# Kernel optimization log

Hardware: AMD Instinct MI355X
Metric: run time of the kernel (lower is better)

The kernel has to match this reference:

```python
import jax, jax.numpy as jnp
import numpy as np

N_SAMPLES = 32768   # exp.n_samples = 2**15
N_FRAMES = 128      # exp.n_frames = n_samples // 256
N_EVENTS = 16
MODEL_DIM = 128
N_FREQS = 16        # 2*16 + 1 = 33 pos-encoding features
POS_DIM = 2 * N_FREQS + 1


def pos_encoded(n_frames, n_freqs):
    # linear position in [-pi, pi] plus sin/cos at geometrically spaced freqs
    x = np.linspace(-np.pi, np.pi, n_frames, dtype=np.float32)[:, None]
    feats = [x]
    for i in range(n_freqs):
        feats.append(np.sin((2.0 ** i) * x))
        feats.append(np.cos((2.0 ** i) * x))
    return jnp.asarray(np.concatenate(feats, axis=-1))  # (n_frames, 33)


def hard_softmax_st(x):
    # softmax -> one-hot at argmax (value forced to exactly 1.0), straight-through backward
    sm = jax.nn.softmax(x, axis=-1)
    onehot = jax.nn.one_hot(jnp.argmax(sm, axis=-1), x.shape[-1], dtype=x.dtype)
    return sm + jax.lax.stop_gradient(onehot - sm)


def fft_convolve(env, tf):
    n = env.shape[-1]
    env = jnp.pad(env, ((0, 0), (0, 0), (0, n)))
    tf = jnp.pad(tf, ((0, 0), (0, 0), (0, n)))
    spec = jnp.fft.rfft(env, axis=-1, norm='ortho') * jnp.fft.rfft(tf, axis=-1, norm='ortho')
    return jnp.fft.irfft(spec, axis=-1, norm='ortho')[..., :n]


def setup_inputs() -> dict:
    key = jax.random.key(0)
    k1, k2, k3, k4, k5 = jax.random.split(key, 5)
    B = 32
    time_latent = jax.random.normal(k1, (B * N_EVENTS, MODEL_DIM), jnp.float32)
    stems = jax.random.normal(k2, (B, N_EVENTS, N_SAMPLES), jnp.float32)
    targets = jax.random.normal(k3, (B, N_EVENTS, N_SAMPLES), jnp.float32)
    lim = 1.0 / np.sqrt(MODEL_DIM)
    W = jax.random.uniform(k4, (MODEL_DIM, POS_DIM), jnp.float32, -lim, lim)
    b = jax.random.uniform(k5, (POS_DIM,), jnp.float32, -lim, lim)
    return {"time_latent": time_latent, "stems": stems, "targets": targets, "W": W, "b": b}


def reference(time_latent, stems, targets, W, b):
    # to_pos linear projection: (B*E, 128) -> (B*E, 33)
    p = time_latent @ W + b
    p = p / (jnp.linalg.norm(p, axis=-1, keepdims=True) + 1e-8)
    pos = pos_encoded(N_FRAMES, N_FREQS)
    pos = pos / (jnp.linalg.norm(pos, axis=-1, keepdims=True) + 1e-8)
    sim = p @ pos.T                      # (B*E, n_frames)
    sm = hard_softmax_st(sim)            # one-hot forward, softmax backward
    step = N_SAMPLES // N_FRAMES         # 256
    sparse = jnp.zeros((p.shape[0], N_SAMPLES), p.dtype).at[:, ::step].set(sm)
    sparse = sparse.reshape(-1, N_EVENTS, N_SAMPLES)  # (B, 16, 32768)
    return fft_convolve(sparse, stems)
```

## Files before the change

kernel.cpp:

```cpp
#include <hip/hip_runtime.h>
#include <math.h>

#define N_SAMPLES 32768
#define N_FRAMES  128
#define N_EVENTS  16
#define MODEL_DIM 128
#define N_FREQS   16
#define POS_DIM   33
#define N_ROWS    512
#define SPLIT     4


__global__ __launch_bounds__(64) void pos_kernel(float* __restrict__ pos_hat) {
    int f = blockIdx.x;
    int j = threadIdx.x;

    __shared__ float s_feat[POS_DIM];
    __shared__ float s_inv;

    double step = (2.0 * M_PI) / 127.0;
    double xd = -M_PI + (double)f * step;
    if (f == N_FRAMES - 1) xd = M_PI;
    float x = (float)xd;

    if (j < POS_DIM) {
        float v;
        if (j == 0) {
            v = x;
        } else {
            int i = (j - 1) >> 1;
            double arg = ldexp((double)x, i);
            v = (j & 1) ? (float)sin(arg) : (float)cos(arg);
        }
        s_feat[j] = v;
    }
    __syncthreads();

    if (j == 0) {
        double nrm = 0.0;
        for (int k = 0; k < POS_DIM; ++k)
            nrm += (double)s_feat[k] * (double)s_feat[k];
        s_inv = 1.0f / ((float)sqrt(nrm) + 1e-8f);
    }
    __syncthreads();

    if (j < POS_DIM) pos_hat[f * POS_DIM + j] = s_feat[j] * s_inv;
}

__global__ __launch_bounds__(1024) void fused_kernel(
    const float* __restrict__ tl,
    const float* __restrict__ W,
    const float* __restrict__ b,
    const float* __restrict__ pos_hat,
    const float* __restrict__ stems,
    float*       __restrict__ out)
{
    __shared__ float  s_tl[MODEL_DIM];
    __shared__ float  s_p[POS_DIM];
    __shared__ double sv[N_FRAMES];
    __shared__ int    si[N_FRAMES];
    __shared__ int    s_d;

    int row = blockIdx.y;
    int t = threadIdx.x;

    if (t < MODEL_DIM) s_tl[t] = tl[(size_t)row * MODEL_DIM + t];
    __syncthreads();

    if (t < POS_DIM) {
        double acc = (double)b[t];
        for (int k = 0; k < MODEL_DIM; ++k)
            acc += (double)s_tl[k] * (double)W[k * POS_DIM + t];
        s_p[t] = (float)acc;
    }
    __syncthreads();

    if (t < N_FRAMES) {
        double s = 0.0;
        for (int j = 0; j < POS_DIM; ++j)
            s += (double)s_p[j] * (double)pos_hat[t * POS_DIM + j];
        sv[t] = s;
        si[t] = t;
    }
    __syncthreads();

    for (int off = 64; off > 0; off >>= 1) {
        if (t < off) {
            double ov = sv[t + off];
            int    oi = si[t + off];
            if (ov > sv[t] || (ov == sv[t] && oi < si[t])) {
                sv[t] = ov;
                si[t] = oi;
            }
        }
        __syncthreads();
    }
    if (t == 0) s_d = si[0] * (N_SAMPLES / N_FRAMES);
    __syncthreads();

    int d = s_d;
    const float4* src = (const float4*)(stems + (size_t)row * N_SAMPLES);
    float4*       dst = (float4*)(out + (size_t)row * N_SAMPLES);
    const float sc = 1.0f / 256.0f;

    int base = blockIdx.x * (N_SAMPLES / SPLIT);
#pragma unroll
    for (int it = 0; it < (N_SAMPLES / SPLIT) / (1024 * 4); ++it) {
        int tt = base + (it * 1024 + t) * 4;
        float4 v;
        if (tt >= d) {
            v = src[(tt - d) >> 2];
            v.x *= sc; v.y *= sc; v.z *= sc; v.w *= sc;
        } else {
            v = make_float4(0.f, 0.f, 0.f, 0.f);
        }
        dst[tt >> 2] = v;
    }
}

extern "C" void kernel_launch(void* const* d_in, const int* in_sizes, int n_in,
                              void* d_out, int out_size, void* d_ws, size_t ws_size,
                              hipStream_t stream) {
    const float* tl    = (const float*)d_in[0];
    const float* stems = (const float*)d_in[1];
    const float* W     = (const float*)d_in[3];
    const float* b     = (const float*)d_in[4];
    float* out = (float*)d_out;

    float* pos_hat = (float*)d_ws;

    pos_kernel<<<N_FRAMES, 64, 0, stream>>>(pos_hat);
    fused_kernel<<<dim3(SPLIT, N_ROWS), 1024, 0, stream>>>(tl, W, b, pos_hat, stems, out);
}
```

Baseline: 182.9 us.

## Hoist per-row projection into setup kernel and shrink shift blocks

The W projection of time_latent is moved out of the per-split shift kernel into the setup kernel, which also builds the position table. Each row is therefore projected once instead of once per split block. The shift kernel now uses 256-thread blocks and twice as many splits per row, so each block finishes its argmax preamble sooner and occupancy is finer-grained. In exchange, p makes an extra round trip through workspace memory and the setup kernel gets larger.

```diff
diff --git a/kernel.cpp b/kernel.cpp
--- a/kernel.cpp
+++ b/kernel.cpp
@@ -8,54 +8,74 @@
 #define N_FREQS   16
 #define POS_DIM   33
 #define N_ROWS    512
-#define SPLIT     4
+#define SPLIT     8
 
+#define WS_P_OFF 17408
 
-__global__ __launch_bounds__(64) void pos_kernel(float* __restrict__ pos_hat) {
-    int f = blockIdx.x;
-    int j = threadIdx.x;
-
-    __shared__ float s_feat[POS_DIM];
-    __shared__ float s_inv;
-
-    double step = (2.0 * M_PI) / 127.0;
-    double xd = -M_PI + (double)f * step;
-    if (f == N_FRAMES - 1) xd = M_PI;
-    float x = (float)xd;
-
-    if (j < POS_DIM) {
-        float v;
-        if (j == 0) {
-            v = x;
-        } else {
-            int i = (j - 1) >> 1;
-            double arg = ldexp((double)x, i);
-            v = (j & 1) ? (float)sin(arg) : (float)cos(arg);
-        }
-        s_feat[j] = v;
-    }
-    __syncthreads();
-
-    if (j == 0) {
-        double nrm = 0.0;
-        for (int k = 0; k < POS_DIM; ++k)
-            nrm += (double)s_feat[k] * (double)s_feat[k];
-        s_inv = 1.0f / ((float)sqrt(nrm) + 1e-8f);
-    }
-    __syncthreads();
-
-    if (j < POS_DIM) pos_hat[f * POS_DIM + j] = s_feat[j] * s_inv;
-}
-
-__global__ __launch_bounds__(1024) void fused_kernel(
+__global__ __launch_bounds__(128) void setup_kernel(
     const float* __restrict__ tl,
     const float* __restrict__ W,
     const float* __restrict__ b,
+    float* __restrict__ pos_hat,
+    float* __restrict__ p_out)
+{
+    int bid = blockIdx.x;
+    int t = threadIdx.x;
+
+    if (bid < N_FRAMES) {
+        int f = bid;
+        __shared__ float s_feat[POS_DIM];
+        __shared__ float s_inv;
+
+        double step = (2.0 * M_PI) / 127.0;
+        double xd = -M_PI + (double)f * step;
+        if (f == N_FRAMES - 1) xd = M_PI;
+        float x = (float)xd;
+
+        if (t < POS_DIM) {
+            float v;
+            if (t == 0) {
+                v = x;
+            } else {
+                int i = (t - 1) >> 1;
+                double arg = ldexp((double)x, i);
+                v = (t & 1) ? (float)sin(arg) : (float)cos(arg);
+            }
+            s_feat[t] = v;
+        }
+        __syncthreads();
+
+        if (t == 0) {
+            double nrm = 0.0;
+            for (int k = 0; k < POS_DIM; ++k)
+                nrm += (double)s_feat[k] * (double)s_feat[k];
+            s_inv = 1.0f / ((float)sqrt(nrm) + 1e-8f);
+        }
+        __syncthreads();
+
+        if (t < POS_DIM) pos_hat[f * POS_DIM + t] = s_feat[t] * s_inv;
+    } else {
+        int row = bid - N_FRAMES;
+        __shared__ float s_tl[MODEL_DIM];
+
+        s_tl[t] = tl[(size_t)row * MODEL_DIM + t];
+        __syncthreads();
+
+        if (t < POS_DIM) {
+            double acc = (double)b[t];
+            for (int k = 0; k < MODEL_DIM; ++k)
+                acc += (double)s_tl[k] * (double)W[k * POS_DIM + t];
+            p_out[row * POS_DIM + t] = (float)acc;
+        }
+    }
+}
+
+__global__ __launch_bounds__(256) void shift_kernel(
+    const float* __restrict__ p,
     const float* __restrict__ pos_hat,
     const float* __restrict__ stems,
     float*       __restrict__ out)
 {
-    __shared__ float  s_tl[MODEL_DIM];
     __shared__ float  s_p[POS_DIM];
     __shared__ double sv[N_FRAMES];
     __shared__ int    si[N_FRAMES];
@@ -64,15 +84,7 @@
     int row = blockIdx.y;
     int t = threadIdx.x;
 
-    if (t < MODEL_DIM) s_tl[t] = tl[(size_t)row * MODEL_DIM + t];
-    __syncthreads();
-
-    if (t < POS_DIM) {
-        double acc = (double)b[t];
-        for (int k = 0; k < MODEL_DIM; ++k)
-            acc += (double)s_tl[k] * (double)W[k * POS_DIM + t];
-        s_p[t] = (float)acc;
-    }
+    if (t < POS_DIM) s_p[t] = p[row * POS_DIM + t];
     __syncthreads();
 
     if (t < N_FRAMES) {
@@ -105,8 +117,8 @@
 
     int base = blockIdx.x * (N_SAMPLES / SPLIT);
 #pragma unroll
-    for (int it = 0; it < (N_SAMPLES / SPLIT) / (1024 * 4); ++it) {
-        int tt = base + (it * 1024 + t) * 4;
+    for (int it = 0; it < (N_SAMPLES / SPLIT) / (256 * 4); ++it) {
+        int tt = base + (it * 256 + t) * 4;
         float4 v;
         if (tt >= d) {
             v = src[(tt - d) >> 2];
@@ -128,7 +140,8 @@
     float* out = (float*)d_out;
 
     float* pos_hat = (float*)d_ws;
+    float* p       = (float*)((char*)d_ws + WS_P_OFF);
 
-    pos_kernel<<<N_FRAMES, 64, 0, stream>>>(pos_hat);
-    fused_kernel<<<dim3(SPLIT, N_ROWS), 1024, 0, stream>>>(tl, W, b, pos_hat, stems, out);
+    setup_kernel<<<N_FRAMES + N_ROWS, 128, 0, stream>>>(tl, W, b, pos_hat, p);
+    shift_kernel<<<dim3(SPLIT, N_ROWS), 256, 0, stream>>>(p, pos_hat, stems, out);
 }
```

After: 175.3 us. -4.2%, faster.
